# Kernel tuning notes

Measured on AMD Instinct MI355X. Metric: run time of the kernel, lower is better.

The kernel has to match this reference:

```python
import jax, jax.numpy as jnp
from jax import lax
import numpy as np

B, CIN, H, W = 8, 3, 512, 512
BASE = 32
TOPK = 200
SCORE_T = 0.01
IOU_T = 0.5
DN = ('NCHW', 'OIHW', 'NCHW')


def setup_inputs() -> dict:
    key = jax.random.key(0)
    ks = jax.random.split(key, 12)
    def conv_w(k, o, i, kh, kw):
        fan_in = i * kh * kw
        return jax.random.normal(k, (o, i, kh, kw), jnp.float32) * (1.0 / np.sqrt(fan_in))
    c = [CIN, BASE, BASE * 2, BASE * 4, BASE * 8]
    inp = {'images': jax.random.normal(ks[0], (B, CIN, H, W), jnp.float32)}
    for l in range(4):
        inp[f'w{l+1}'] = conv_w(ks[1 + 2 * l], c[l + 1], c[l], 3, 3)
        inp[f'b{l+1}'] = jnp.zeros((c[l + 1],), jnp.float32)
    inp['wh'] = conv_w(ks[9], 5, c[4], 1, 1)
    inp['bh'] = jnp.zeros((5,), jnp.float32)
    return inp


def _conv_relu_pool(x, w, b):
    x = lax.conv_general_dilated(x, w, (1, 1), 'SAME', dimension_numbers=DN)
    x = jax.nn.relu(x + b[None, :, None, None])
    return lax.reduce_window(x, -jnp.inf, lax.max, (1, 1, 2, 2), (1, 1, 2, 2), 'VALID')


def _decode(pred):
    # pred: [B,5,Gh,Gw]
    Bn, _, Gh, Gw = pred.shape
    sy, sx = H / float(Gh), W / float(Gw)
    obj = jax.nn.sigmoid(pred[:, 0])
    tx = jax.nn.sigmoid(pred[:, 1])
    ty = jax.nn.sigmoid(pred[:, 2])
    bw = jnp.exp(pred[:, 3]) * sx
    bh = jnp.exp(pred[:, 4]) * sy
    gy = jnp.arange(Gh, dtype=pred.dtype)[None, :, None]
    gx = jnp.arange(Gw, dtype=pred.dtype)[None, None, :]
    cx = gx * sx + tx * sx
    cy = gy * sy + ty * sy
    x1 = jnp.clip(cx - bw / 2.0, 0.0, W - 1)
    y1 = jnp.clip(cy - bh / 2.0, 0.0, H - 1)
    x2 = jnp.clip(cx + bw / 2.0, 0.0, W - 1)
    y2 = jnp.clip(cy + bh / 2.0, 0.0, H - 1)
    boxes = jnp.stack([x1, y1, x2, y2], axis=-1).reshape(Bn, Gh * Gw, 4)
    scores = obj.reshape(Bn, Gh * Gw)
    # score threshold + top-k (fixed size, padded with invalid entries)
    masked = jnp.where(scores >= SCORE_T, scores, -1.0)
    svals, sidx = lax.top_k(masked, TOPK)                      # [B,K]
    boxes_k = jnp.take_along_axis(boxes, sidx[:, :, None], axis=1)  # [B,K,4]
    valid = svals >= SCORE_T
    # pairwise IoU [B,K,K]
    bx1, by1, bx2, by2 = (boxes_k[..., i] for i in range(4))
    area = (bx2 - bx1) * (by2 - by1)
    xx1 = jnp.maximum(bx1[:, :, None], bx1[:, None, :])
    yy1 = jnp.maximum(by1[:, :, None], by1[:, None, :])
    xx2 = jnp.minimum(bx2[:, :, None], bx2[:, None, :])
    yy2 = jnp.minimum(by2[:, :, None], by2[:, None, :])
    inter = jnp.clip(xx2 - xx1, 0.0) * jnp.clip(yy2 - yy1, 0.0)
    union = area[:, :, None] + area[:, None, :] - inter
    iou = inter / jnp.maximum(union, 1e-6)
    ar = jnp.arange(TOPK)
    def body(i, keep):  # greedy NMS over score-sorted boxes
        sup = (iou[:, i, :] > IOU_T) & (ar[None, :] > i) & keep[:, i][:, None]
        return keep & ~sup
    keep = lax.fori_loop(0, TOPK, body, valid)
    scores_k = jnp.where(valid, svals, 0.0)
    return boxes_k, scores_k, keep


def reference(images, w1, b1, w2, b2, w3, b3, w4, b4, wh, bh):
    x = _conv_relu_pool(images, w1, b1)
    x = _conv_relu_pool(x, w2, b2)
    x = _conv_relu_pool(x, w3, b3)
    x = _conv_relu_pool(x, w4, b4)
    pred = lax.conv_general_dilated(x, wh, (1, 1), 'SAME', dimension_numbers=DN)
    pred = pred + bh[None, :, None, None]
    boxes, scores, keep = _decode(pred)
    kf = keep.astype(boxes.dtype)
    out5 = jnp.concatenate([boxes, scores[..., None]], axis=-1) * kf[..., None]
    return out5, keep
```

## Files before the change

### kernel.cpp

```cpp
#include <hip/hip_runtime.h>
#include <math.h>


constexpr int TOPK_N = 200;

typedef double f64x4 __attribute__((ext_vector_type(4)));

template <int CIN, int CI_BLK, int CO_BLK>
__launch_bounds__(256)
__global__ void conv_relu_pool_pipe(const float* __restrict__ in,
                                    const float* __restrict__ wgt,
                                    const float* __restrict__ bias,
                                    float* __restrict__ out,
                                    int Hin, int Win, int Cout) {
    constexpr int SPATIAL = 34 * 34;
    constexpr int SSLOT = (SPATIAL + 255) / 256;
    constexpr int NW = CI_BLK * 9 * CO_BLK;
    constexpr int NCHUNK = CIN / CI_BLK;
    const int Hp = Hin >> 1, Wp = Win >> 1;
    const int coChunks = Cout / CO_BLK;
    const int b  = blockIdx.z / coChunks;
    const int cz = blockIdx.z % coChunks;
    const int tid = threadIdx.x;
    const int tx = tid & 15, ty = tid >> 4;
    const int px = (blockIdx.x << 4) + tx;
    const int py = (blockIdx.y << 4) + ty;
    const int iy0 = (blockIdx.y << 5) - 1;
    const int ix0 = (blockIdx.x << 5) - 1;

    __shared__ float  s_in[2][CI_BLK * SPATIAL];
    __shared__ double s_w[2][NW];

    int soff[SSLOT];
#pragma unroll
    for (int s = 0; s < SSLOT; ++s) {
        const int cell = tid + s * 256;
        int g = -1;
        if (cell < SPATIAL) {
            const int ly = cell / 34, lx = cell - ly * 34;
            const int iy = iy0 + ly, ix = ix0 + lx;
            if ((unsigned)iy < (unsigned)Hin && (unsigned)ix < (unsigned)Win)
                g = iy * Win + ix;
        }
        soff[s] = g;
    }
    int wg = -1;
    if (tid < NW) {
        const int co   = tid & (CO_BLK - 1);
        const int rest = tid / CO_BLK;
        const int k    = rest % 9;
        const int ci   = rest / 9;
        wg = ((cz * CO_BLK + co) * CIN + ci) * 9 + k;
    }
    const size_t HW = (size_t)Hin * Win;
    const float* in_b = in + (size_t)b * CIN * HW;

    double acc[CO_BLK][4];
#pragma unroll
    for (int co = 0; co < CO_BLK; ++co)
#pragma unroll
        for (int p = 0; p < 4; ++p) acc[co][p] = 0.0;

    float rin[CI_BLK][SSLOT];
    float rw = 0.f;

#pragma unroll
    for (int ci = 0; ci < CI_BLK; ++ci) {
        const float* src = in_b + ci * HW;
#pragma unroll
        for (int s = 0; s < SSLOT; ++s) {
            const int cell = tid + s * 256;
            float v = 0.f;
            if (cell < SPATIAL) { const int g = soff[s]; if (g >= 0) v = src[g]; }
            rin[ci][s] = v;
        }
    }
    if (tid < NW) rw = wgt[wg];
#pragma unroll
    for (int ci = 0; ci < CI_BLK; ++ci)
#pragma unroll
        for (int s = 0; s < SSLOT; ++s) {
            const int cell = tid + s * 256;
            if (cell < SPATIAL) s_in[0][ci * SPATIAL + cell] = rin[ci][s];
        }
    if (tid < NW) s_w[0][tid] = (double)rw;
    __syncthreads();

    for (int c = 0; c < NCHUNK; ++c) {
        const int buf = c & 1;
        if (c + 1 < NCHUNK) {
            const int c0n = (c + 1) * CI_BLK;
#pragma unroll
            for (int ci = 0; ci < CI_BLK; ++ci) {
                const float* src = in_b + (c0n + ci) * HW;
#pragma unroll
                for (int s = 0; s < SSLOT; ++s) {
                    const int cell = tid + s * 256;
                    float v = 0.f;
                    if (cell < SPATIAL) { const int g = soff[s]; if (g >= 0) v = src[g]; }
                    rin[ci][s] = v;
                }
            }
            if (tid < NW) rw = wgt[wg + c0n * 9];
        }
#pragma unroll 1
        for (int ci = 0; ci < CI_BLK; ++ci) {
            const float* tile = &s_in[buf][ci * SPATIAL];
            double win[4][4];
#pragma unroll
            for (int iy = 0; iy < 4; ++iy) {
                float2 r0 = *(const float2*)&tile[(2 * ty + iy) * 34 + 2 * tx];
                float2 r1 = *(const float2*)&tile[(2 * ty + iy) * 34 + 2 * tx + 2];
                win[iy][0] = (double)r0.x; win[iy][1] = (double)r0.y;
                win[iy][2] = (double)r1.x; win[iy][3] = (double)r1.y;
            }
#pragma unroll
            for (int k = 0; k < 9; ++k) {
                const int ky = k / 3, kx = k % 3;
                const double* wp = &s_w[buf][(ci * 9 + k) * CO_BLK];
                double w[CO_BLK];
#pragma unroll
                for (int co = 0; co < CO_BLK; ++co) w[co] = wp[co];
#pragma unroll
                for (int p = 0; p < 4; ++p) {
                    const double v = win[(p >> 1) + ky][(p & 1) + kx];
#pragma unroll
                    for (int co = 0; co < CO_BLK; ++co)
                        acc[co][p] = fma(v, w[co], acc[co][p]);
                }
            }
        }
        if (c + 1 < NCHUNK) {
#pragma unroll
            for (int ci = 0; ci < CI_BLK; ++ci)
#pragma unroll
                for (int s = 0; s < SSLOT; ++s) {
                    const int cell = tid + s * 256;
                    if (cell < SPATIAL) s_in[buf ^ 1][ci * SPATIAL + cell] = rin[ci][s];
                }
            if (tid < NW) s_w[buf ^ 1][tid] = (double)rw;
            __syncthreads();
        }
    }

#pragma unroll
    for (int co = 0; co < CO_BLK; ++co) {
        const double bd = (double)bias[cz * CO_BLK + co];
        const float e0 = fmaxf((float)(acc[co][0] + bd), 0.f);
        const float e1 = fmaxf((float)(acc[co][1] + bd), 0.f);
        const float e2 = fmaxf((float)(acc[co][2] + bd), 0.f);
        const float e3 = fmaxf((float)(acc[co][3] + bd), 0.f);
        out[((size_t)(b * Cout + cz * CO_BLK + co) * Hp + py) * Wp + px] =
            fmaxf(fmaxf(e0, e1), fmaxf(e2, e3));
    }
}

template <int CIN>
__launch_bounds__(256, 2)
__global__ void conv_mfma_f64(const float* __restrict__ in,
                              const float* __restrict__ wgt,
                              const float* __restrict__ bias,
                              float* __restrict__ out,
                              int Hin, int Win, int Cout) {
    constexpr int TW = 34;
    constexpr int CELLS = 34 * 10;
    constexpr int CH = 360;
    constexpr int CI_CHUNK = 8;
    constexpr int NCHUNK = CIN / CI_CHUNK;
    constexpr int WST = 296;

    const int Hp = Hin >> 1, Wp = Win >> 1;
    const int coChunks = Cout >> 5;
    const int b   = blockIdx.z / coChunks;
    const int cob = blockIdx.z % coChunks;
    const int tid = threadIdx.x;
    const int wv  = tid >> 6;
    const int l15 = tid & 15;
    const int l4  = (tid >> 4) & 3;
    const int x0 = blockIdx.x << 5;
    const int y0 = blockIdx.y << 3;

    __shared__ float  s_in[2][CI_CHUNK * CH];
    __shared__ double s_w[2][CI_CHUNK * WST];

    int soff[2];
#pragma unroll
    for (int s = 0; s < 2; ++s) {
        const int cell = tid + s * 256;
        int g = -1;
        if (cell < CELLS) {
            const int ly = cell / TW, lx = cell - ly * TW;
            const int iy = y0 - 1 + ly, ix = x0 - 1 + lx;
            if ((unsigned)iy < (unsigned)Hin && (unsigned)ix < (unsigned)Win)
                g = iy * Win + ix;
        }
        soff[s] = g;
    }
    int wgoff[9], lwoff[9];
#pragma unroll
    for (int s = 0; s < 9; ++s) {
        const int idx  = s * 256 + tid;
        const int co_l = idx & 31;
        const int r    = idx >> 5;
        const int tap  = r % 9;
        const int ci_l = r / 9;
        wgoff[s] = ((cob * 32 + co_l) * CIN + ci_l) * 9 + tap;
        lwoff[s] = ci_l * WST + tap * 32 + co_l;
    }
    const size_t HW = (size_t)Hin * Win;
    const float* in_b = in + (size_t)b * CIN * HW;

    int abase[4];
#pragma unroll
    for (int m = 0; m < 4; ++m) {
        const int dy = m >> 1, xh = m & 1;
        abase[m] = l4 * CH + (2 * wv + dy) * TW + xh * 16 + l15;
    }
    const int bbase0 = l4 * WST + l15;
    const int bbase1 = l4 * WST + 16 + l15;

    f64x4 acc[4][2];
#pragma unroll
    for (int m = 0; m < 4; ++m)
#pragma unroll
        for (int n = 0; n < 2; ++n)
#pragma unroll
            for (int j = 0; j < 4; ++j) acc[m][n][j] = 0.0;

    float rin[CI_CHUNK][2];
    float rwt[9];

#pragma unroll
    for (int ci = 0; ci < CI_CHUNK; ++ci) {
        const float* src = in_b + (size_t)ci * HW;
        rin[ci][0] = (soff[0] >= 0) ? src[soff[0]] : 0.f;
        rin[ci][1] = (soff[1] >= 0) ? src[soff[1]] : 0.f;
    }
#pragma unroll
    for (int s = 0; s < 9; ++s) rwt[s] = wgt[wgoff[s]];
#pragma unroll
    for (int ci = 0; ci < CI_CHUNK; ++ci) {
        s_in[0][ci * CH + tid] = rin[ci][0];
        if (tid < CELLS - 256) s_in[0][ci * CH + tid + 256] = rin[ci][1];
    }
#pragma unroll
    for (int s = 0; s < 9; ++s) s_w[0][lwoff[s]] = (double)rwt[s];
    __syncthreads();

#define R18_KA(kk) ((((kk)&1) * 4 * CH) + ((((kk)>>1) / 3) * TW) + (((kk)>>1) % 3))
#define R18_KB(kk) ((((kk)&1) * 4 * WST) + (((kk)>>1) * 32))

#pragma unroll 2
    for (int c = 0; c < NCHUNK; ++c) {
        const int buf = c & 1;
        if (c + 1 < NCHUNK) {
            const int c0n = (c + 1) * CI_CHUNK;
#pragma unroll
            for (int ci = 0; ci < CI_CHUNK; ++ci) {
                const float* src = in_b + (size_t)(c0n + ci) * HW;
                rin[ci][0] = (soff[0] >= 0) ? src[soff[0]] : 0.f;
                rin[ci][1] = (soff[1] >= 0) ? src[soff[1]] : 0.f;
            }
#pragma unroll
            for (int s = 0; s < 9; ++s) rwt[s] = wgt[wgoff[s] + c0n * 9];
        }
        {
            const float*  ti = &s_in[buf][0];
            const double* tw = &s_w[buf][0];
            double A0, A1, A2, A3, B0, B1;
            B0 = tw[bbase0 + R18_KB(0)];
            B1 = tw[bbase1 + R18_KB(0)];
            A0 = (double)ti[abase[0] + R18_KA(0)];
            A1 = (double)ti[abase[1] + R18_KA(0)];
            A2 = (double)ti[abase[2] + R18_KA(0)];
            A3 = (double)ti[abase[3] + R18_KA(0)];
#pragma unroll
            for (int kk = 0; kk < 18; ++kk) {
                double nA0, nA1, nA2, nA3, nB0, nB1;
                if (kk + 1 < 18) {
                    nB0 = tw[bbase0 + R18_KB(kk + 1)];
                    nB1 = tw[bbase1 + R18_KB(kk + 1)];
                    nA0 = (double)ti[abase[0] + R18_KA(kk + 1)];
                    nA1 = (double)ti[abase[1] + R18_KA(kk + 1)];
                    nA2 = (double)ti[abase[2] + R18_KA(kk + 1)];
                    nA3 = (double)ti[abase[3] + R18_KA(kk + 1)];
                }
                acc[0][0] = __builtin_amdgcn_mfma_f64_16x16x4f64(A0, B0, acc[0][0], 0, 0, 0);
                acc[0][1] = __builtin_amdgcn_mfma_f64_16x16x4f64(A0, B1, acc[0][1], 0, 0, 0);
                acc[1][0] = __builtin_amdgcn_mfma_f64_16x16x4f64(A1, B0, acc[1][0], 0, 0, 0);
                acc[1][1] = __builtin_amdgcn_mfma_f64_16x16x4f64(A1, B1, acc[1][1], 0, 0, 0);
                acc[2][0] = __builtin_amdgcn_mfma_f64_16x16x4f64(A2, B0, acc[2][0], 0, 0, 0);
                acc[2][1] = __builtin_amdgcn_mfma_f64_16x16x4f64(A2, B1, acc[2][1], 0, 0, 0);
                acc[3][0] = __builtin_amdgcn_mfma_f64_16x16x4f64(A3, B0, acc[3][0], 0, 0, 0);
                acc[3][1] = __builtin_amdgcn_mfma_f64_16x16x4f64(A3, B1, acc[3][1], 0, 0, 0);
                if (kk + 1 < 18) {
                    A0 = nA0; A1 = nA1; A2 = nA2; A3 = nA3;
                    B0 = nB0; B1 = nB1;
                }
            }
        }
        if (c + 1 < NCHUNK) {
#pragma unroll
            for (int ci = 0; ci < CI_CHUNK; ++ci) {
                s_in[buf ^ 1][ci * CH + tid] = rin[ci][0];
                if (tid < CELLS - 256) s_in[buf ^ 1][ci * CH + tid + 256] = rin[ci][1];
            }
#pragma unroll
            for (int s = 0; s < 9; ++s) s_w[buf ^ 1][lwoff[s]] = (double)rwt[s];
            __syncthreads();
        }
    }
#undef R18_KA
#undef R18_KB

    const int yp = (y0 >> 1) + wv;
#pragma unroll
    for (int n = 0; n < 2; ++n) {
        const int co = cob * 32 + n * 16 + l15;
        const double bd = (double)bias[co];
        float* orow = out + (((size_t)b * Cout + co) * Hp + yp) * Wp;
#pragma unroll
        for (int xh = 0; xh < 2; ++xh) {
#pragma unroll
            for (int r = 0; r < 4; ++r) {
                const float e0 = fmaxf((float)(acc[xh][n][r]     + bd), 0.f);
                const float e1 = fmaxf((float)(acc[2 + xh][n][r] + bd), 0.f);
                float v = fmaxf(e0, e1);
                const float p = __shfl_xor(v, 16, 64);
                v = fmaxf(v, p);
                if ((l4 & 1) == 0) {
                    const int xp = (x0 >> 1) + xh * 8 + 2 * r + (l4 >> 1);
                    orow[xp] = v;
                }
            }
        }
    }
}

__launch_bounds__(256)
__global__ void head_decode_k(const float* __restrict__ x4,
                              const float* __restrict__ wh,
                              const float* __restrict__ bh,
                              float* __restrict__ boxes,
                              float* __restrict__ scores) {
    __shared__ float s_wh[5 * 256];
    const int tid = threadIdx.x;
#pragma unroll
    for (int i = 0; i < 5; ++i) s_wh[i * 256 + tid] = wh[i * 256 + tid];
    __syncthreads();

    const int idx  = blockIdx.x * 256 + tid;
    const int b    = idx >> 10;
    const int cell = idx & 1023;
    const int gy = cell >> 5, gx = cell & 31;

    double a0 = (double)bh[0], a1 = (double)bh[1], a2 = (double)bh[2],
           a3 = (double)bh[3], a4 = (double)bh[4];
    const float* xp = x4 + b * 262144 + cell;
    for (int ci = 0; ci < 256; ++ci) {
        const double v = (double)xp[ci << 10];
        a0 = fma(v, (double)s_wh[0 * 256 + ci], a0);
        a1 = fma(v, (double)s_wh[1 * 256 + ci], a1);
        a2 = fma(v, (double)s_wh[2 * 256 + ci], a2);
        a3 = fma(v, (double)s_wh[3 * 256 + ci], a3);
        a4 = fma(v, (double)s_wh[4 * 256 + ci], a4);
    }
    const double obj = 1.0 / (1.0 + exp(-a0));
    const double txs = 1.0 / (1.0 + exp(-a1));
    const double tys = 1.0 / (1.0 + exp(-a2));
    const double bw  = exp(a3) * 16.0;
    const double bhh = exp(a4) * 16.0;
    const double cx  = gx * 16.0 + txs * 16.0;
    const double cy  = gy * 16.0 + tys * 16.0;
    float* bp = boxes + idx * 4;
    bp[0] = (float)fmin(fmax(cx - bw * 0.5, 0.0), 511.0);
    bp[1] = (float)fmin(fmax(cy - bhh * 0.5, 0.0), 511.0);
    bp[2] = (float)fmin(fmax(cx + bw * 0.5, 0.0), 511.0);
    bp[3] = (float)fmin(fmax(cy + bhh * 0.5, 0.0), 511.0);
    scores[idx] = (float)obj;
}

__launch_bounds__(256)
__global__ void topk_nms_k(const float* __restrict__ boxes,
                           const float* __restrict__ scores,
                           float* __restrict__ out5,
                           float* __restrict__ keep_out) {
    const int b = blockIdx.x, tid = threadIdx.x;
    __shared__ unsigned long long key[1024];
    __shared__ float bx1[TOPK_N], by1[TOPK_N], bx2[TOPK_N], by2[TOPK_N];
    __shared__ float sv[TOPK_N], ar[TOPK_N];
    __shared__ int   kp[TOPK_N];

    for (int i = tid; i < 1024; i += 256) {
        float s = scores[b * 1024 + i];
        float m = (s >= 0.01f) ? s : -1.0f;
        unsigned u = __float_as_uint(m);
        u = (u & 0x80000000u) ? ~u : (u | 0x80000000u);
        key[i] = ((unsigned long long)u << 32) | (unsigned)(1023 - i);
    }
    __syncthreads();

    for (int k = 2; k <= 1024; k <<= 1) {
        for (int j = k >> 1; j > 0; j >>= 1) {
            for (int i = tid; i < 1024; i += 256) {
                int l = i ^ j;
                if (l > i) {
                    unsigned long long a = key[i], c = key[l];
                    bool desc = ((i & k) == 0);
                    bool sw = desc ? (a < c) : (a > c);
                    if (sw) { key[i] = c; key[l] = a; }
                }
            }
            __syncthreads();
        }
    }

    for (int i = tid; i < TOPK_N; i += 256) {
        unsigned long long kk = key[i];
        unsigned u = (unsigned)(kk >> 32);
        unsigned bits = (u & 0x80000000u) ? (u & 0x7FFFFFFFu) : ~u;
        float s = __uint_as_float(bits);
        int src = 1023 - (int)(kk & 0xFFFFFFFFu);
        const float4 bb = *(const float4*)(boxes + (b * 1024 + src) * 4);
        bx1[i] = bb.x; by1[i] = bb.y; bx2[i] = bb.z; by2[i] = bb.w;
        sv[i] = s;
        ar[i] = (bb.z - bb.x) * (bb.w - bb.y);
        kp[i] = (s >= 0.01f) ? 1 : 0;
    }
    __syncthreads();

    for (int i = 0; i < TOPK_N; ++i) {
        if (kp[i]) {
            const float X1 = bx1[i], Y1 = by1[i], X2 = bx2[i], Y2 = by2[i], A = ar[i];
            for (int j = tid; j < TOPK_N; j += 256) {
                if (j > i && kp[j]) {
                    float xx1 = fmaxf(X1, bx1[j]);
                    float yy1 = fmaxf(Y1, by1[j]);
                    float xx2 = fminf(X2, bx2[j]);
                    float yy2 = fminf(Y2, by2[j]);
                    float inter = fmaxf(xx2 - xx1, 0.f) * fmaxf(yy2 - yy1, 0.f);
                    float uni = A + ar[j] - inter;
                    float iou = inter / fmaxf(uni, 1e-6f);
                    if (iou > 0.5f) kp[j] = 0;
                }
            }
        }
        __syncthreads();
    }

    for (int i = tid; i < TOPK_N; i += 256) {
        float kf = kp[i] ? 1.f : 0.f;
        float s  = sv[i];
        float sc = (s >= 0.01f) ? s : 0.f;
        float* op = out5 + (b * TOPK_N + i) * 5;
        op[0] = bx1[i] * kf;
        op[1] = by1[i] * kf;
        op[2] = bx2[i] * kf;
        op[3] = by2[i] * kf;
        op[4] = sc * kf;
        keep_out[b * TOPK_N + i] = kf;
    }
}

extern "C" void kernel_launch(void* const* d_in, const int* in_sizes, int n_in,
                              void* d_out, int out_size, void* d_ws, size_t ws_size,
                              hipStream_t stream) {
    const float* images = (const float*)d_in[0];
    const float* w1 = (const float*)d_in[1];
    const float* b1 = (const float*)d_in[2];
    const float* w2 = (const float*)d_in[3];
    const float* b2 = (const float*)d_in[4];
    const float* w3 = (const float*)d_in[5];
    const float* b3 = (const float*)d_in[6];
    const float* w4 = (const float*)d_in[7];
    const float* b4 = (const float*)d_in[8];
    const float* wh = (const float*)d_in[9];
    const float* bh = (const float*)d_in[10];
    float* out = (float*)d_out;

    float* A    = (float*)d_ws;
    float* Bbuf = A + 16777216;
    float* boxes  = A + 8388608;
    float* scores = A + 8388608 + 32768;

    conv_relu_pool_pipe<3, 3, 8><<<dim3(16, 16, 8 * 4), 256, 0, stream>>>(
        images, w1, b1, A, 512, 512, 32);
    conv_mfma_f64<32><<<dim3(8, 32, 8 * 2), 256, 0, stream>>>(
        A, w2, b2, Bbuf, 256, 256, 64);
    conv_mfma_f64<64><<<dim3(4, 16, 8 * 4), 256, 0, stream>>>(
        Bbuf, w3, b3, A, 128, 128, 128);
    conv_mfma_f64<128><<<dim3(2, 8, 8 * 8), 256, 0, stream>>>(
        A, w4, b4, Bbuf, 64, 64, 256);
    head_decode_k<<<32, 256, 0, stream>>>(Bbuf, wh, bh, boxes, scores);
    topk_nms_k<<<8, 256, 0, stream>>>(boxes, scores, out, out + 8 * TOPK_N * 5);
}
```

Measured before the change: 1.213 ms.

## Split conv blocks between FP64 MFMA and vector FMA paths by output-channel parity

Convolution layers 2-4 now run on a flattened 1D grid. Blocks are interleaved in runs of 256, and alternate runs take one of two roles. Role-0 blocks keep the FP64 MFMA path, while role-1 blocks compute their output-channel chunk with scalar FP64 FMAs from a 32-entry register accumulator per thread. The aim is to use both the matrix and vector FP64 pipes at the same time across co-resident blocks. The cost is a register-heavy vector path that can spill or cut occupancy, and the two roles may run at different speeds and unbalance the load.

```diff
diff --git a/kernel.cpp b/kernel.cpp
--- a/kernel.cpp
+++ b/kernel.cpp
@@ -157,7 +157,7 @@
 
 template <int CIN>
 __launch_bounds__(256, 2)
-__global__ void conv_mfma_f64(const float* __restrict__ in,
+__global__ void conv_dual_f64(const float* __restrict__ in,
                               const float* __restrict__ wgt,
                               const float* __restrict__ bias,
                               float* __restrict__ out,
@@ -171,14 +171,23 @@
 
     const int Hp = Hin >> 1, Wp = Win >> 1;
     const int coChunks = Cout >> 5;
-    const int b   = blockIdx.z / coChunks;
-    const int cob = blockIdx.z % coChunks;
+    const int gx = Win >> 5, gy = Hin >> 3;
+    const int chHalf = coChunks >> 1;
+
+    const int L    = (int)blockIdx.x;
+    const int run  = L >> 8;
+    const int role = run & 1;
+    const int T    = (L & 255) | ((run >> 1) << 8);
+    int t = T;
+    const int bx = t % gx;  t /= gx;
+    const int by = t % gy;  t /= gy;
+    const int ch = t % chHalf;
+    const int b  = t / chHalf;
+    const int cob = (ch << 1) | role;
+
     const int tid = threadIdx.x;
-    const int wv  = tid >> 6;
-    const int l15 = tid & 15;
-    const int l4  = (tid >> 4) & 3;
-    const int x0 = blockIdx.x << 5;
-    const int y0 = blockIdx.y << 3;
+    const int x0 = bx << 5;
+    const int y0 = by << 3;
 
     __shared__ float  s_in[2][CI_CHUNK * CH];
     __shared__ double s_w[2][CI_CHUNK * WST];
@@ -210,128 +219,231 @@
     const size_t HW = (size_t)Hin * Win;
     const float* in_b = in + (size_t)b * CIN * HW;
 
-    int abase[4];
-#pragma unroll
-    for (int m = 0; m < 4; ++m) {
-        const int dy = m >> 1, xh = m & 1;
-        abase[m] = l4 * CH + (2 * wv + dy) * TW + xh * 16 + l15;
-    }
-    const int bbase0 = l4 * WST + l15;
-    const int bbase1 = l4 * WST + 16 + l15;
-
-    f64x4 acc[4][2];
-#pragma unroll
-    for (int m = 0; m < 4; ++m)
-#pragma unroll
-        for (int n = 0; n < 2; ++n)
-#pragma unroll
-            for (int j = 0; j < 4; ++j) acc[m][n][j] = 0.0;
-
-    float rin[CI_CHUNK][2];
-    float rwt[9];
-
-#pragma unroll
-    for (int ci = 0; ci < CI_CHUNK; ++ci) {
-        const float* src = in_b + (size_t)ci * HW;
-        rin[ci][0] = (soff[0] >= 0) ? src[soff[0]] : 0.f;
-        rin[ci][1] = (soff[1] >= 0) ? src[soff[1]] : 0.f;
-    }
-#pragma unroll
-    for (int s = 0; s < 9; ++s) rwt[s] = wgt[wgoff[s]];
-#pragma unroll
-    for (int ci = 0; ci < CI_CHUNK; ++ci) {
-        s_in[0][ci * CH + tid] = rin[ci][0];
-        if (tid < CELLS - 256) s_in[0][ci * CH + tid + 256] = rin[ci][1];
-    }
-#pragma unroll
-    for (int s = 0; s < 9; ++s) s_w[0][lwoff[s]] = (double)rwt[s];
-    __syncthreads();
-
-#define R18_KA(kk) ((((kk)&1) * 4 * CH) + ((((kk)>>1) / 3) * TW) + (((kk)>>1) % 3))
-#define R18_KB(kk) ((((kk)&1) * 4 * WST) + (((kk)>>1) * 32))
-
+    if (role == 0) {
+        const int wv  = tid >> 6;
+        const int l15 = tid & 15;
+        const int l4  = (tid >> 4) & 3;
+        int abase[4];
+#pragma unroll
+        for (int m = 0; m < 4; ++m) {
+            const int dy = m >> 1, xh = m & 1;
+            abase[m] = l4 * CH + (2 * wv + dy) * TW + xh * 16 + l15;
+        }
+        const int bbase0 = l4 * WST + l15;
+        const int bbase1 = l4 * WST + 16 + l15;
+
+        f64x4 acc[4][2];
+#pragma unroll
+        for (int m = 0; m < 4; ++m)
+#pragma unroll
+            for (int n = 0; n < 2; ++n)
+#pragma unroll
+                for (int j = 0; j < 4; ++j) acc[m][n][j] = 0.0;
+
+        float rin[CI_CHUNK][2];
+        float rwt[9];
+
+#pragma unroll
+        for (int ci = 0; ci < CI_CHUNK; ++ci) {
+            const float* src = in_b + (size_t)ci * HW;
+            rin[ci][0] = (soff[0] >= 0) ? src[soff[0]] : 0.f;
+            rin[ci][1] = (soff[1] >= 0) ? src[soff[1]] : 0.f;
+        }
+#pragma unroll
+        for (int s = 0; s < 9; ++s) rwt[s] = wgt[wgoff[s]];
+#pragma unroll
+        for (int ci = 0; ci < CI_CHUNK; ++ci) {
+            s_in[0][ci * CH + tid] = rin[ci][0];
+            if (tid < CELLS - 256) s_in[0][ci * CH + tid + 256] = rin[ci][1];
+        }
+#pragma unroll
+        for (int s = 0; s < 9; ++s) s_w[0][lwoff[s]] = (double)rwt[s];
+        __syncthreads();
+
+#define R19_KA(kk) ((((kk)&1) * 4 * CH) + ((((kk)>>1) / 3) * TW) + (((kk)>>1) % 3))
+#define R19_KB(kk) ((((kk)&1) * 4 * WST) + (((kk)>>1) * 32))
 #pragma unroll 2
-    for (int c = 0; c < NCHUNK; ++c) {
-        const int buf = c & 1;
-        if (c + 1 < NCHUNK) {
-            const int c0n = (c + 1) * CI_CHUNK;
-#pragma unroll
-            for (int ci = 0; ci < CI_CHUNK; ++ci) {
-                const float* src = in_b + (size_t)(c0n + ci) * HW;
-                rin[ci][0] = (soff[0] >= 0) ? src[soff[0]] : 0.f;
-                rin[ci][1] = (soff[1] >= 0) ? src[soff[1]] : 0.f;
-            }
-#pragma unroll
-            for (int s = 0; s < 9; ++s) rwt[s] = wgt[wgoff[s] + c0n * 9];
-        }
-        {
-            const float*  ti = &s_in[buf][0];
-            const double* tw = &s_w[buf][0];
-            double A0, A1, A2, A3, B0, B1;
-            B0 = tw[bbase0 + R18_KB(0)];
-            B1 = tw[bbase1 + R18_KB(0)];
-            A0 = (double)ti[abase[0] + R18_KA(0)];
-            A1 = (double)ti[abase[1] + R18_KA(0)];
-            A2 = (double)ti[abase[2] + R18_KA(0)];
-            A3 = (double)ti[abase[3] + R18_KA(0)];
-#pragma unroll
-            for (int kk = 0; kk < 18; ++kk) {
-                double nA0, nA1, nA2, nA3, nB0, nB1;
-                if (kk + 1 < 18) {
-                    nB0 = tw[bbase0 + R18_KB(kk + 1)];
-                    nB1 = tw[bbase1 + R18_KB(kk + 1)];
-                    nA0 = (double)ti[abase[0] + R18_KA(kk + 1)];
-                    nA1 = (double)ti[abase[1] + R18_KA(kk + 1)];
-                    nA2 = (double)ti[abase[2] + R18_KA(kk + 1)];
-                    nA3 = (double)ti[abase[3] + R18_KA(kk + 1)];
-                }
-                acc[0][0] = __builtin_amdgcn_mfma_f64_16x16x4f64(A0, B0, acc[0][0], 0, 0, 0);
-                acc[0][1] = __builtin_amdgcn_mfma_f64_16x16x4f64(A0, B1, acc[0][1], 0, 0, 0);
-                acc[1][0] = __builtin_amdgcn_mfma_f64_16x16x4f64(A1, B0, acc[1][0], 0, 0, 0);
-                acc[1][1] = __builtin_amdgcn_mfma_f64_16x16x4f64(A1, B1, acc[1][1], 0, 0, 0);
-                acc[2][0] = __builtin_amdgcn_mfma_f64_16x16x4f64(A2, B0, acc[2][0], 0, 0, 0);
-                acc[2][1] = __builtin_amdgcn_mfma_f64_16x16x4f64(A2, B1, acc[2][1], 0, 0, 0);
-                acc[3][0] = __builtin_amdgcn_mfma_f64_16x16x4f64(A3, B0, acc[3][0], 0, 0, 0);
-                acc[3][1] = __builtin_amdgcn_mfma_f64_16x16x4f64(A3, B1, acc[3][1], 0, 0, 0);
-                if (kk + 1 < 18) {
-                    A0 = nA0; A1 = nA1; A2 = nA2; A3 = nA3;
-                    B0 = nB0; B1 = nB1;
-                }
-            }
-        }
-        if (c + 1 < NCHUNK) {
-#pragma unroll
-            for (int ci = 0; ci < CI_CHUNK; ++ci) {
-                s_in[buf ^ 1][ci * CH + tid] = rin[ci][0];
-                if (tid < CELLS - 256) s_in[buf ^ 1][ci * CH + tid + 256] = rin[ci][1];
-            }
-#pragma unroll
-            for (int s = 0; s < 9; ++s) s_w[buf ^ 1][lwoff[s]] = (double)rwt[s];
-            __syncthreads();
-        }
-    }
-#undef R18_KA
-#undef R18_KB
-
-    const int yp = (y0 >> 1) + wv;
-#pragma unroll
-    for (int n = 0; n < 2; ++n) {
-        const int co = cob * 32 + n * 16 + l15;
-        const double bd = (double)bias[co];
-        float* orow = out + (((size_t)b * Cout + co) * Hp + yp) * Wp;
-#pragma unroll
-        for (int xh = 0; xh < 2; ++xh) {
-#pragma unroll
-            for (int r = 0; r < 4; ++r) {
-                const float e0 = fmaxf((float)(acc[xh][n][r]     + bd), 0.f);
-                const float e1 = fmaxf((float)(acc[2 + xh][n][r] + bd), 0.f);
-                float v = fmaxf(e0, e1);
-                const float p = __shfl_xor(v, 16, 64);
-                v = fmaxf(v, p);
-                if ((l4 & 1) == 0) {
-                    const int xp = (x0 >> 1) + xh * 8 + 2 * r + (l4 >> 1);
-                    orow[xp] = v;
-                }
+        for (int c = 0; c < NCHUNK; ++c) {
+            const int buf = c & 1;
+            if (c + 1 < NCHUNK) {
+                const int c0n = (c + 1) * CI_CHUNK;
+#pragma unroll
+                for (int ci = 0; ci < CI_CHUNK; ++ci) {
+                    const float* src = in_b + (size_t)(c0n + ci) * HW;
+                    rin[ci][0] = (soff[0] >= 0) ? src[soff[0]] : 0.f;
+                    rin[ci][1] = (soff[1] >= 0) ? src[soff[1]] : 0.f;
+                }
+#pragma unroll
+                for (int s = 0; s < 9; ++s) rwt[s] = wgt[wgoff[s] + c0n * 9];
+            }
+            {
+                const float*  ti = &s_in[buf][0];
+                const double* tw = &s_w[buf][0];
+                double A0, A1, A2, A3, B0, B1;
+                B0 = tw[bbase0 + R19_KB(0)];
+                B1 = tw[bbase1 + R19_KB(0)];
+                A0 = (double)ti[abase[0] + R19_KA(0)];
+                A1 = (double)ti[abase[1] + R19_KA(0)];
+                A2 = (double)ti[abase[2] + R19_KA(0)];
+                A3 = (double)ti[abase[3] + R19_KA(0)];
+#pragma unroll
+                for (int kk = 0; kk < 18; ++kk) {
+                    double nA0, nA1, nA2, nA3, nB0, nB1;
+                    if (kk + 1 < 18) {
+                        nB0 = tw[bbase0 + R19_KB(kk + 1)];
+                        nB1 = tw[bbase1 + R19_KB(kk + 1)];
+                        nA0 = (double)ti[abase[0] + R19_KA(kk + 1)];
+                        nA1 = (double)ti[abase[1] + R19_KA(kk + 1)];
+                        nA2 = (double)ti[abase[2] + R19_KA(kk + 1)];
+                        nA3 = (double)ti[abase[3] + R19_KA(kk + 1)];
+                    }
+                    acc[0][0] = __builtin_amdgcn_mfma_f64_16x16x4f64(A0, B0, acc[0][0], 0, 0, 0);
+                    acc[0][1] = __builtin_amdgcn_mfma_f64_16x16x4f64(A0, B1, acc[0][1], 0, 0, 0);
+                    acc[1][0] = __builtin_amdgcn_mfma_f64_16x16x4f64(A1, B0, acc[1][0], 0, 0, 0);
+                    acc[1][1] = __builtin_amdgcn_mfma_f64_16x16x4f64(A1, B1, acc[1][1], 0, 0, 0);
+                    acc[2][0] = __builtin_amdgcn_mfma_f64_16x16x4f64(A2, B0, acc[2][0], 0, 0, 0);
+                    acc[2][1] = __builtin_amdgcn_mfma_f64_16x16x4f64(A2, B1, acc[2][1], 0, 0, 0);
+                    acc[3][0] = __builtin_amdgcn_mfma_f64_16x16x4f64(A3, B0, acc[3][0], 0, 0, 0);
+                    acc[3][1] = __builtin_amdgcn_mfma_f64_16x16x4f64(A3, B1, acc[3][1], 0, 0, 0);
+                    if (kk + 1 < 18) {
+                        A0 = nA0; A1 = nA1; A2 = nA2; A3 = nA3;
+                        B0 = nB0; B1 = nB1;
+                    }
+                }
+            }
+            if (c + 1 < NCHUNK) {
+#pragma unroll
+                for (int ci = 0; ci < CI_CHUNK; ++ci) {
+                    s_in[buf ^ 1][ci * CH + tid] = rin[ci][0];
+                    if (tid < CELLS - 256) s_in[buf ^ 1][ci * CH + tid + 256] = rin[ci][1];
+                }
+#pragma unroll
+                for (int s = 0; s < 9; ++s) s_w[buf ^ 1][lwoff[s]] = (double)rwt[s];
+                __syncthreads();
+            }
+        }
+#undef R19_KA
+#undef R19_KB
+
+        const int yp = (y0 >> 1) + wv;
+#pragma unroll
+        for (int n = 0; n < 2; ++n) {
+            const int co = cob * 32 + n * 16 + l15;
+            const double bd = (double)bias[co];
+            float* orow = out + (((size_t)b * Cout + co) * Hp + yp) * Wp;
+#pragma unroll
+            for (int xh = 0; xh < 2; ++xh) {
+#pragma unroll
+                for (int r = 0; r < 4; ++r) {
+                    const float e0 = fmaxf((float)(acc[xh][n][r]     + bd), 0.f);
+                    const float e1 = fmaxf((float)(acc[2 + xh][n][r] + bd), 0.f);
+                    float v = fmaxf(e0, e1);
+                    const float p = __shfl_xor(v, 16, 64);
+                    v = fmaxf(v, p);
+                    if ((l4 & 1) == 0) {
+                        const int xp = (x0 >> 1) + xh * 8 + 2 * r + (l4 >> 1);
+                        orow[xp] = v;
+                    }
+                }
+            }
+        }
+    } else {
+        const int co = tid & 31;
+        const int yy = tid >> 5;
+
+        double vacc[32];
+#pragma unroll
+        for (int x = 0; x < 32; ++x) vacc[x] = 0.0;
+
+        float rin[CI_CHUNK][2];
+        float rwt[9];
+
+#pragma unroll
+        for (int ci = 0; ci < CI_CHUNK; ++ci) {
+            const float* src = in_b + (size_t)ci * HW;
+            rin[ci][0] = (soff[0] >= 0) ? src[soff[0]] : 0.f;
+            rin[ci][1] = (soff[1] >= 0) ? src[soff[1]] : 0.f;
+        }
+#pragma unroll
+        for (int s = 0; s < 9; ++s) rwt[s] = wgt[wgoff[s]];
+#pragma unroll
+        for (int ci = 0; ci < CI_CHUNK; ++ci) {
+            s_in[0][ci * CH + tid] = rin[ci][0];
+            if (tid < CELLS - 256) s_in[0][ci * CH + tid + 256] = rin[ci][1];
+        }
+#pragma unroll
+        for (int s = 0; s < 9; ++s) s_w[0][lwoff[s]] = (double)rwt[s];
+        __syncthreads();
+
+#pragma unroll 1
+        for (int c = 0; c < NCHUNK; ++c) {
+            const int buf = c & 1;
+            if (c + 1 < NCHUNK) {
+                const int c0n = (c + 1) * CI_CHUNK;
+#pragma unroll
+                for (int ci = 0; ci < CI_CHUNK; ++ci) {
+                    const float* src = in_b + (size_t)(c0n + ci) * HW;
+                    rin[ci][0] = (soff[0] >= 0) ? src[soff[0]] : 0.f;
+                    rin[ci][1] = (soff[1] >= 0) ? src[soff[1]] : 0.f;
+                }
+#pragma unroll
+                for (int s = 0; s < 9; ++s) rwt[s] = wgt[wgoff[s] + c0n * 9];
+            }
+            {
+                const float*  ti = &s_in[buf][0];
+                const double* tw = &s_w[buf][0];
+#pragma unroll 1
+                for (int ci = 0; ci < CI_CHUNK; ++ci) {
+                    const float*  trow = ti + ci * CH;
+                    const double* wrow = tw + ci * WST;
+#pragma unroll
+                    for (int ky = 0; ky < 3; ++ky) {
+                        double rv[34];
+#pragma unroll
+                        for (int xx = 0; xx < 34; ++xx)
+                            rv[xx] = (double)trow[(yy + ky) * TW + xx];
+#pragma unroll
+                        for (int kx = 0; kx < 3; ++kx) {
+                            const double w = wrow[(ky * 3 + kx) * 32 + co];
+#pragma unroll
+                            for (int xx = 0; xx < 32; ++xx)
+                                vacc[xx] = fma(rv[xx + kx], w, vacc[xx]);
+                        }
+                    }
+                }
+            }
+            if (c + 1 < NCHUNK) {
+#pragma unroll
+                for (int ci = 0; ci < CI_CHUNK; ++ci) {
+                    s_in[buf ^ 1][ci * CH + tid] = rin[ci][0];
+                    if (tid < CELLS - 256) s_in[buf ^ 1][ci * CH + tid + 256] = rin[ci][1];
+                }
+#pragma unroll
+                for (int s = 0; s < 9; ++s) s_w[buf ^ 1][lwoff[s]] = (double)rwt[s];
+                __syncthreads();
+            }
+        }
+
+        const int gco = cob * 32 + co;
+        const double bd = (double)bias[gco];
+        float pv[16];
+#pragma unroll
+        for (int k = 0; k < 16; ++k) {
+            const float e0 = fmaxf((float)(vacc[2 * k]     + bd), 0.f);
+            const float e1 = fmaxf((float)(vacc[2 * k + 1] + bd), 0.f);
+            float p = fmaxf(e0, e1);
+            const float q = __shfl_xor(p, 32, 64);
+            pv[k] = fmaxf(p, q);
+        }
+        if ((yy & 1) == 0) {
+            const int ypv = (y0 >> 1) + (yy >> 1);
+            float* orow = out + (((size_t)b * Cout + gco) * Hp + ypv) * Wp + (x0 >> 1);
+#pragma unroll
+            for (int k = 0; k < 4; ++k) {
+                float4 v4;
+                v4.x = pv[4 * k];     v4.y = pv[4 * k + 1];
+                v4.z = pv[4 * k + 2]; v4.w = pv[4 * k + 3];
+                *(float4*)&orow[4 * k] = v4;
             }
         }
     }
@@ -485,11 +597,11 @@
 
     conv_relu_pool_pipe<3, 3, 8><<<dim3(16, 16, 8 * 4), 256, 0, stream>>>(
         images, w1, b1, A, 512, 512, 32);
-    conv_mfma_f64<32><<<dim3(8, 32, 8 * 2), 256, 0, stream>>>(
+    conv_dual_f64<32><<<dim3(4096), 256, 0, stream>>>(
         A, w2, b2, Bbuf, 256, 256, 64);
-    conv_mfma_f64<64><<<dim3(4, 16, 8 * 4), 256, 0, stream>>>(
+    conv_dual_f64<64><<<dim3(2048), 256, 0, stream>>>(
         Bbuf, w3, b3, A, 128, 128, 128);
-    conv_mfma_f64<128><<<dim3(2, 8, 8 * 8), 256, 0, stream>>>(
+    conv_dual_f64<128><<<dim3(1024), 256, 0, stream>>>(
         A, w4, b4, Bbuf, 64, 64, 256);
     head_decode_k<<<32, 256, 0, stream>>>(Bbuf, wh, bh, boxes, scores);
     topk_nms_k<<<8, 256, 0, stream>>>(boxes, scores, out, out + 8 * TOPK_N * 5);
```

New measurement: 1.531 ms. 1.26x slower.

## Double channel chunk per barrier and store conv weights as float in LDS

Applied to the files above, without the earlier changes.

The MFMA f64 conv kernel now stages 16 input channels per double-buffered step instead of 8, halving the number of barriers and global-load rounds. Weights are kept as float in shared memory and converted to double at use, which halves LDS weight space so the larger chunk still fits. The weight-load index mapping is rewritten for the larger chunk, and the outer loop is no longer unrolled. In exchange, more registers are held for prefetched inputs and weights, which may lower occupancy or cause spills.

```diff
diff --git a/kernel.cpp b/kernel.cpp
--- a/kernel.cpp
+++ b/kernel.cpp
@@ -164,10 +164,11 @@
                               int Hin, int Win, int Cout) {
     constexpr int TW = 34;
     constexpr int CELLS = 34 * 10;
-    constexpr int CH = 360;
-    constexpr int CI_CHUNK = 8;
+    constexpr int CH = 344;
+    constexpr int CI_CHUNK = 16;
     constexpr int NCHUNK = CIN / CI_CHUNK;
     constexpr int WST = 296;
+    constexpr int NWS = CI_CHUNK * 9 * 32 / 256;
 
     const int Hp = Hin >> 1, Wp = Win >> 1;
     const int coChunks = Cout >> 5;
@@ -180,8 +181,8 @@
     const int x0 = blockIdx.x << 5;
     const int y0 = blockIdx.y << 3;
 
-    __shared__ float  s_in[2][CI_CHUNK * CH];
-    __shared__ double s_w[2][CI_CHUNK * WST];
+    __shared__ float s_in[2][CI_CHUNK * CH];
+    __shared__ float s_w[2][CI_CHUNK * WST];
 
     int soff[2];
 #pragma unroll
@@ -196,17 +197,10 @@
         }
         soff[s] = g;
     }
-    int wgoff[9], lwoff[9];
-#pragma unroll
-    for (int s = 0; s < 9; ++s) {
-        const int idx  = s * 256 + tid;
-        const int co_l = idx & 31;
-        const int r    = idx >> 5;
-        const int tap  = r % 9;
-        const int ci_l = r / 9;
-        wgoff[s] = ((cob * 32 + co_l) * CIN + ci_l) * 9 + tap;
-        lwoff[s] = ci_l * WST + tap * 32 + co_l;
-    }
+    const int co_l = tid & 31;
+    const int r8   = tid >> 5;
+    const int wbase = (cob * 32 + co_l) * CIN * 9;
+
     const size_t HW = (size_t)Hin * Win;
     const float* in_b = in + (size_t)b * CIN * HW;
 
@@ -228,7 +222,7 @@
             for (int j = 0; j < 4; ++j) acc[m][n][j] = 0.0;
 
     float rin[CI_CHUNK][2];
-    float rwt[9];
+    float rwt[NWS];
 
 #pragma unroll
     for (int ci = 0; ci < CI_CHUNK; ++ci) {
@@ -237,20 +231,28 @@
         rin[ci][1] = (soff[1] >= 0) ? src[soff[1]] : 0.f;
     }
 #pragma unroll
-    for (int s = 0; s < 9; ++s) rwt[s] = wgt[wgoff[s]];
+    for (int s = 0; s < NWS; ++s) {
+        const int r = s * 8 + r8;
+        const int tap = r % 9, ci = r / 9;
+        rwt[s] = wgt[wbase + ci * 9 + tap];
+    }
 #pragma unroll
     for (int ci = 0; ci < CI_CHUNK; ++ci) {
         s_in[0][ci * CH + tid] = rin[ci][0];
         if (tid < CELLS - 256) s_in[0][ci * CH + tid + 256] = rin[ci][1];
     }
 #pragma unroll
-    for (int s = 0; s < 9; ++s) s_w[0][lwoff[s]] = (double)rwt[s];
+    for (int s = 0; s < NWS; ++s) {
+        const int r = s * 8 + r8;
+        const int tap = r % 9, ci = r / 9;
+        s_w[0][ci * WST + tap * 32 + co_l] = rwt[s];
+    }
     __syncthreads();
 
-#define R18_KA(kk) ((((kk)&1) * 4 * CH) + ((((kk)>>1) / 3) * TW) + (((kk)>>1) % 3))
-#define R18_KB(kk) ((((kk)&1) * 4 * WST) + (((kk)>>1) * 32))
-
-#pragma unroll 2
+#define R20_KA(kk) ((((kk)&1) * 4 * CH) + ((((kk)>>1) / 3) * TW) + (((kk)>>1) % 3))
+#define R20_KB(kk) ((((kk)&1) * 4 * WST) + (((kk)>>1) * 32))
+
+#pragma unroll 1
     for (int c = 0; c < NCHUNK; ++c) {
         const int buf = c & 1;
         if (c + 1 < NCHUNK) {
@@ -262,28 +264,33 @@
                 rin[ci][1] = (soff[1] >= 0) ? src[soff[1]] : 0.f;
             }
 #pragma unroll
-            for (int s = 0; s < 9; ++s) rwt[s] = wgt[wgoff[s] + c0n * 9];
-        }
-        {
-            const float*  ti = &s_in[buf][0];
-            const double* tw = &s_w[buf][0];
+            for (int s = 0; s < NWS; ++s) {
+                const int r = s * 8 + r8;
+                const int tap = r % 9, ci = r / 9;
+                rwt[s] = wgt[wbase + (c0n + ci) * 9 + tap];
+            }
+        }
+#pragma unroll
+        for (int h = 0; h < 2; ++h) {
+            const float* ti = &s_in[buf][h * 8 * CH];
+            const float* tw = &s_w[buf][h * 8 * WST];
             double A0, A1, A2, A3, B0, B1;
-            B0 = tw[bbase0 + R18_KB(0)];
-            B1 = tw[bbase1 + R18_KB(0)];
-            A0 = (double)ti[abase[0] + R18_KA(0)];
-            A1 = (double)ti[abase[1] + R18_KA(0)];
-            A2 = (double)ti[abase[2] + R18_KA(0)];
-            A3 = (double)ti[abase[3] + R18_KA(0)];
+            B0 = (double)tw[bbase0 + R20_KB(0)];
+            B1 = (double)tw[bbase1 + R20_KB(0)];
+            A0 = (double)ti[abase[0] + R20_KA(0)];
+            A1 = (double)ti[abase[1] + R20_KA(0)];
+            A2 = (double)ti[abase[2] + R20_KA(0)];
+            A3 = (double)ti[abase[3] + R20_KA(0)];
 #pragma unroll
             for (int kk = 0; kk < 18; ++kk) {
                 double nA0, nA1, nA2, nA3, nB0, nB1;
                 if (kk + 1 < 18) {
-                    nB0 = tw[bbase0 + R18_KB(kk + 1)];
-                    nB1 = tw[bbase1 + R18_KB(kk + 1)];
-                    nA0 = (double)ti[abase[0] + R18_KA(kk + 1)];
-                    nA1 = (double)ti[abase[1] + R18_KA(kk + 1)];
-                    nA2 = (double)ti[abase[2] + R18_KA(kk + 1)];
-                    nA3 = (double)ti[abase[3] + R18_KA(kk + 1)];
+                    nB0 = (double)tw[bbase0 + R20_KB(kk + 1)];
+                    nB1 = (double)tw[bbase1 + R20_KB(kk + 1)];
+                    nA0 = (double)ti[abase[0] + R20_KA(kk + 1)];
+                    nA1 = (double)ti[abase[1] + R20_KA(kk + 1)];
+                    nA2 = (double)ti[abase[2] + R20_KA(kk + 1)];
+                    nA3 = (double)ti[abase[3] + R20_KA(kk + 1)];
                 }
                 acc[0][0] = __builtin_amdgcn_mfma_f64_16x16x4f64(A0, B0, acc[0][0], 0, 0, 0);
                 acc[0][1] = __builtin_amdgcn_mfma_f64_16x16x4f64(A0, B1, acc[0][1], 0, 0, 0);
@@ -306,12 +313,16 @@
                 if (tid < CELLS - 256) s_in[buf ^ 1][ci * CH + tid + 256] = rin[ci][1];
             }
 #pragma unroll
-            for (int s = 0; s < 9; ++s) s_w[buf ^ 1][lwoff[s]] = (double)rwt[s];
+            for (int s = 0; s < NWS; ++s) {
+                const int r = s * 8 + r8;
+                const int tap = r % 9, ci = r / 9;
+                s_w[buf ^ 1][ci * WST + tap * 32 + co_l] = rwt[s];
+            }
             __syncthreads();
         }
     }
-#undef R18_KA
-#undef R18_KB
+#undef R20_KA
+#undef R20_KB
 
     const int yp = (y0 >> 1) + wv;
 #pragma unroll
```

Result: slower. 1.360 ms (+12.1%).
